# Kernel tuning notes

Hardware: AMD Instinct MI355X
Metric: run time of the kernel (lower is better)

Reference implementation:

```python
import jax, jax.numpy as jnp
import numpy as np

N_CTRL_U = 64
N_CTRL_V = 64
N_EVAL = 2001  # int(1/0.0005) + 1


def _clamped_knots(p, n_ctrl, dtype):
    """Clamped uniform knot vector on [0,1], length n_ctrl + p + 1."""
    n_internal = n_ctrl - p - 1
    internal = jnp.linspace(0.0, 1.0, n_internal + 2, dtype=dtype)[1:-1]
    return jnp.concatenate([
        jnp.zeros(p + 1, dtype=dtype), internal, jnp.ones(p + 1, dtype=dtype)
    ])


def _find_spans(knots, u, p, n_ctrl):
    """Knot-span index for each parameter (NURBS book A2.1, via searchsorted)."""
    return jnp.clip(jnp.searchsorted(knots, u, side='right') - 1, p, n_ctrl - 1)


def _basis_functions(knots, spans, u, p):
    """Cox-de-Boor nonzero basis functions (NURBS book A2.2), vectorized over u.
    Returns [N, p+1]."""
    Ns = [jnp.ones_like(u)]
    left = {}
    right = {}
    for j in range(1, p + 1):
        left[j] = u - knots[spans + 1 - j]
        right[j] = knots[spans + j] - u
        saved = jnp.zeros_like(u)
        new = []
        for r in range(j):
            temp = Ns[r] / (right[r + 1] + left[j - r])
            new.append(saved + right[r + 1] * temp)
            saved = left[j - r] * temp
        new.append(saved)
        Ns = new
    return jnp.stack(Ns, axis=-1)


def setup_inputs() -> dict:
    key = jax.random.key(0)
    k1, = jax.random.split(key, 1)
    control_points = jax.random.normal(k1, (N_CTRL_U, N_CTRL_V, 3), dtype=jnp.float32)
    params_u = jnp.linspace(0.0, 1.0, N_EVAL, dtype=jnp.float32)
    params_v = jnp.linspace(0.0, 1.0, N_EVAL, dtype=jnp.float32)
    return {"control_points": control_points, "params_u": params_u,
            "params_v": params_v, "degree": 3}


def reference(control_points, params_u, params_v, degree):
    p = int(degree)
    n_u, n_v, d = control_points.shape
    dt = control_points.dtype
    ku = _clamped_knots(p, n_u, dt)
    kv = _clamped_knots(p, n_v, dt)
    su = _find_spans(ku, params_u, p, n_u)          # [Nu]
    sv = _find_spans(kv, params_v, p, n_v)          # [Nv]
    Bu = _basis_functions(ku, su, params_u, p)      # [Nu, p+1]
    Bv = _basis_functions(kv, sv, params_v, p)      # [Nv, p+1]
    off = jnp.arange(p + 1)
    iu = su[:, None] - p + off[None, :]             # [Nu, p+1]
    iv = sv[:, None] - p + off[None, :]             # [Nv, p+1]
    # Contract u first to keep intermediates small: [Nu, p+1, n_v, d] -> [Nu, n_v, d]
    ctrl_u = control_points[iu]                     # gather rows by span
    curve_u = jnp.einsum('ua,uavd->uvd', Bu, ctrl_u)
    # Gather v spans then contract: [Nu, Nv, p+1, d] -> [Nu, Nv, d]
    pts = curve_u[:, iv]
    return jnp.einsum('vb,uvbd->uvd', Bv, pts)
```

## Files before the change

kernel.cpp:

```cpp
#include <hip/hip_runtime.h>

#define N_EVAL 2001
#define NCTRL  64

__device__ __forceinline__ float knotv(int i) {
    if (i <= 3) return 0.0f;
    if (i >= NCTRL) return 1.0f;
    return (float)(i - 3) * (1.0f / 61.0f);
}

__device__ __forceinline__ void basis_p3(float u, int& span, float4& N) {
    int s = 3 + (int)floorf(u * 61.0f);
    s = max(3, min(63, s));
    while (s < 63 && knotv(s + 1) <= u) ++s;
    while (s > 3 && knotv(s) > u) --s;

    float left[4], right[4], Ns[4];
    Ns[0] = 1.0f;
    #pragma unroll
    for (int j = 1; j <= 3; ++j) {
        left[j]  = u - knotv(s + 1 - j);
        right[j] = knotv(s + j) - u;
        float saved = 0.0f;
        #pragma unroll
        for (int r = 0; r < j; ++r) {
            float temp = Ns[r] / (right[r + 1] + left[j - r]);
            Ns[r] = saved + right[r + 1] * temp;
            saved = left[j - r] * temp;
        }
        Ns[j] = saved;
    }
    span = s;
    N = make_float4(Ns[0], Ns[1], Ns[2], Ns[3]);
}

__global__ void basis_kernel(const float* __restrict__ pu, const float* __restrict__ pv,
                             float4* __restrict__ Bu, float4* __restrict__ Bv,
                             int* __restrict__ su, int* __restrict__ sv) {
    int gid = blockIdx.x * blockDim.x + threadIdx.x;
    if (gid < 2048) {
        if (gid < N_EVAL) {
            int s; float4 N;
            basis_p3(pu[gid], s, N);
            Bu[gid] = N; su[gid] = s;
        }
    } else {
        int i = gid - 2048;
        if (i < N_EVAL) {
            int s; float4 N;
            basis_p3(pv[i], s, N);
            Bv[i] = N; sv[i] = s;
        }
    }
}

__global__ __launch_bounds__(256) void eval_kernel(const float* __restrict__ cp,
                                                   const float4* __restrict__ Bu,
                                                   const float4* __restrict__ Bv,
                                                   const int* __restrict__ su,
                                                   const int* __restrict__ sv,
                                                   float* __restrict__ out) {
    __shared__ float4 curve[NCTRL];
    __shared__ float  stage[768];

    const int u = blockIdx.x;
    const int t = threadIdx.x;
    const int s_u = su[u];
    const float4 bu = Bu[u];

    if (t < NCTRL * 3) {
        const int base = (s_u - 3) * (NCTRL * 3);
        float c = bu.x * cp[base +       t]
                + bu.y * cp[base + 192 + t]
                + bu.z * cp[base + 384 + t]
                + bu.w * cp[base + 576 + t];
        int j = t / 3, d = t - 3 * j;
        ((float*)curve)[j * 4 + d] = c;
    }
    __syncthreads();

    float* orow = out + (size_t)u * (N_EVAL * 3);

    #pragma unroll
    for (int k = 0; k < 8; ++k) {
        const int v = k * 256 + t;
        float x = 0.f, y = 0.f, z = 0.f;
        if (v < N_EVAL) {
            const float4 bv = Bv[v];
            const int iv0 = sv[v] - 3;
            float4 c0 = curve[iv0 + 0];
            float4 c1 = curve[iv0 + 1];
            float4 c2 = curve[iv0 + 2];
            float4 c3 = curve[iv0 + 3];
            x = bv.x * c0.x + bv.y * c1.x + bv.z * c2.x + bv.w * c3.x;
            y = bv.x * c0.y + bv.y * c1.y + bv.z * c2.y + bv.w * c3.y;
            z = bv.x * c0.z + bv.y * c1.z + bv.z * c2.z + bv.w * c3.z;
        }
        if (k) __syncthreads();
        if (v < N_EVAL) {
            stage[3 * t + 0] = x;
            stage[3 * t + 1] = y;
            stage[3 * t + 2] = z;
        }
        __syncthreads();
        const int rowbase = k * 768;
        #pragma unroll
        for (int j = 0; j < 3; ++j) {
            int idx = j * 256 + t;
            if (rowbase + idx < N_EVAL * 3)
                orow[rowbase + idx] = stage[idx];
        }
    }
}

extern "C" void kernel_launch(void* const* d_in, const int* in_sizes, int n_in,
                              void* d_out, int out_size, void* d_ws, size_t ws_size,
                              hipStream_t stream) {
    const float* cp = (const float*)d_in[0];
    const float* pu = (const float*)d_in[1];
    const float* pv = (const float*)d_in[2];
    float* out = (float*)d_out;

    float4* Bu = (float4*)d_ws;
    float4* Bv = Bu + 2048;
    int* su = (int*)(Bu + 4096);
    int* sv = su + 2048;

    basis_kernel<<<16, 256, 0, stream>>>(pu, pv, Bu, Bv, su, sv);
    eval_kernel<<<N_EVAL, 256, 0, stream>>>(cp, Bu, Bv, su, sv, out);
}
```

Measured before the change: 83.05 us.

## Fuse basis computation into eval kernel and vectorize aligned row stores

Drops the separate basis kernel: each block computes its u basis inline, and every thread recomputes its v basis per element rather than loading precomputed values. The output staging buffer is double-buffered, which removes one barrier per iteration, and it is shifted so each row can be written with aligned float4 stores plus scalar head and tail writes. Division is replaced by the hardware reciprocal. The cost is redundant basis arithmetic across 2001 blocks, and the approximate reciprocal may change numerics slightly.

```diff
diff --git a/kernel.cpp b/kernel.cpp
--- a/kernel.cpp
+++ b/kernel.cpp
@@ -2,6 +2,7 @@
 
 #define N_EVAL 2001
 #define NCTRL  64
+#define ROWF   (N_EVAL * 3)
 
 __device__ __forceinline__ float knotv(int i) {
     if (i <= 3) return 0.0f;
@@ -24,7 +25,7 @@
         float saved = 0.0f;
         #pragma unroll
         for (int r = 0; r < j; ++r) {
-            float temp = Ns[r] / (right[r + 1] + left[j - r]);
+            float temp = Ns[r] * __builtin_amdgcn_rcpf(right[r + 1] + left[j - r]);
             Ns[r] = saved + right[r + 1] * temp;
             saved = left[j - r] * temp;
         }
@@ -34,39 +35,18 @@
     N = make_float4(Ns[0], Ns[1], Ns[2], Ns[3]);
 }
 
-__global__ void basis_kernel(const float* __restrict__ pu, const float* __restrict__ pv,
-                             float4* __restrict__ Bu, float4* __restrict__ Bv,
-                             int* __restrict__ su, int* __restrict__ sv) {
-    int gid = blockIdx.x * blockDim.x + threadIdx.x;
-    if (gid < 2048) {
-        if (gid < N_EVAL) {
-            int s; float4 N;
-            basis_p3(pu[gid], s, N);
-            Bu[gid] = N; su[gid] = s;
-        }
-    } else {
-        int i = gid - 2048;
-        if (i < N_EVAL) {
-            int s; float4 N;
-            basis_p3(pv[i], s, N);
-            Bv[i] = N; sv[i] = s;
-        }
-    }
-}
-
 __global__ __launch_bounds__(256) void eval_kernel(const float* __restrict__ cp,
-                                                   const float4* __restrict__ Bu,
-                                                   const float4* __restrict__ Bv,
-                                                   const int* __restrict__ su,
-                                                   const int* __restrict__ sv,
+                                                   const float* __restrict__ pu,
+                                                   const float* __restrict__ pv,
                                                    float* __restrict__ out) {
     __shared__ float4 curve[NCTRL];
-    __shared__ float  stage[768];
+    __shared__ float  stage[2][776];
 
     const int u = blockIdx.x;
     const int t = threadIdx.x;
-    const int s_u = su[u];
-    const float4 bu = Bu[u];
+
+    int s_u; float4 bu;
+    basis_p3(pu[u], s_u, bu);
 
     if (t < NCTRL * 3) {
         const int base = (s_u - 3) * (NCTRL * 3);
@@ -79,15 +59,17 @@
     }
     __syncthreads();
 
-    float* orow = out + (size_t)u * (N_EVAL * 3);
+    const size_t rowstart = (size_t)u * ROWF;
+    const int shift    = (int)(rowstart & 3);
+    const int slotbase = shift ? 4 : 0;
 
-    #pragma unroll
     for (int k = 0; k < 8; ++k) {
         const int v = k * 256 + t;
         float x = 0.f, y = 0.f, z = 0.f;
         if (v < N_EVAL) {
-            const float4 bv = Bv[v];
-            const int iv0 = sv[v] - 3;
+            int s_v; float4 bv;
+            basis_p3(pv[v], s_v, bv);
+            const int iv0 = s_v - 3;
             float4 c0 = curve[iv0 + 0];
             float4 c1 = curve[iv0 + 1];
             float4 c2 = curve[iv0 + 2];
@@ -96,19 +78,33 @@
             y = bv.x * c0.y + bv.y * c1.y + bv.z * c2.y + bv.w * c3.y;
             z = bv.x * c0.z + bv.y * c1.z + bv.z * c2.z + bv.w * c3.z;
         }
-        if (k) __syncthreads();
+        float* st = stage[k & 1];
         if (v < N_EVAL) {
-            stage[3 * t + 0] = x;
-            stage[3 * t + 1] = y;
-            stage[3 * t + 2] = z;
+            st[3 * t + 0 + shift] = x;
+            st[3 * t + 1 + shift] = y;
+            st[3 * t + 2 + shift] = z;
         }
         __syncthreads();
-        const int rowbase = k * 768;
-        #pragma unroll
-        for (int j = 0; j < 3; ++j) {
-            int idx = j * 256 + t;
-            if (rowbase + idx < N_EVAL * 3)
-                orow[rowbase + idx] = stage[idx];
+
+        const int    g0    = k * 768;
+        const int    cnt   = (g0 + 768 <= ROWF) ? 768 : (ROWF - g0);
+        const size_t gabs0 = rowstart + g0;
+        const int    head  = (4 - shift) & 3;
+        const int    nf    = (cnt - head) >> 2;
+
+        if (t < nf) {
+            float4 q = *reinterpret_cast<const float4*>(&st[slotbase + 4 * t]);
+            reinterpret_cast<float4*>(out + gabs0 + head)[t] = q;
+        }
+        if (t >= 240 && t < 240 + head) {
+            int h = t - 240;
+            out[gabs0 + h] = st[shift + h];
+        }
+        const int done  = head + 4 * nf;
+        const int tailc = cnt - done;
+        if (t >= 244 && t < 244 + tailc) {
+            int h = t - 244;
+            out[gabs0 + done + h] = st[shift + done + h];
         }
     }
 }
@@ -121,11 +117,5 @@
     const float* pv = (const float*)d_in[2];
     float* out = (float*)d_out;
 
-    float4* Bu = (float4*)d_ws;
-    float4* Bv = Bu + 2048;
-    int* su = (int*)(Bu + 4096);
-    int* sv = su + 2048;
-
-    basis_kernel<<<16, 256, 0, stream>>>(pu, pv, Bu, Bv, su, sv);
-    eval_kernel<<<N_EVAL, 256, 0, stream>>>(cp, Bu, Bv, su, sv, out);
+    eval_kernel<<<N_EVAL, 256, 0, stream>>>(cp, pu, pv, out);
 }
```

Result: slower. 93.58 us (+12.7%).

## Write output rows with aligned float4 stores and pack v-basis with span

Applied to the files above, without the earlier changes.

Each output row is now written as aligned float4 vectors. Each thread recomputes the two points that straddle its 16-byte slot, and a few threads fill the unaligned head and tail elements, so the shared-memory staging buffer and its barriers go away. The v-basis is packed into one float4 holding three weights plus the span, with the fourth weight rebuilt as one minus the sum, which removes a separate span load. The cost is roughly double the point evaluations and a small floating-point difference in the rebuilt weight.

```diff
diff --git a/kernel.cpp b/kernel.cpp
--- a/kernel.cpp
+++ b/kernel.cpp
@@ -2,6 +2,7 @@
 
 #define N_EVAL 2001
 #define NCTRL  64
+#define ROWF   6003
 
 __device__ __forceinline__ float knotv(int i) {
     if (i <= 3) return 0.0f;
@@ -9,13 +10,12 @@
     return (float)(i - 3) * (1.0f / 61.0f);
 }
 
-__device__ __forceinline__ void basis_p3(float u, int& span, float4& N) {
+__device__ __forceinline__ void basis_p3(float u, int& span, float* Ns) {
     int s = 3 + (int)floorf(u * 61.0f);
     s = max(3, min(63, s));
     while (s < 63 && knotv(s + 1) <= u) ++s;
     while (s > 3 && knotv(s) > u) --s;
-
-    float left[4], right[4], Ns[4];
+    float left[4], right[4];
     Ns[0] = 1.0f;
     #pragma unroll
     for (int j = 1; j <= 3; ++j) {
@@ -31,42 +31,45 @@
         Ns[j] = saved;
     }
     span = s;
-    N = make_float4(Ns[0], Ns[1], Ns[2], Ns[3]);
 }
 
 __global__ void basis_kernel(const float* __restrict__ pu, const float* __restrict__ pv,
-                             float4* __restrict__ Bu, float4* __restrict__ Bv,
-                             int* __restrict__ su, int* __restrict__ sv) {
+                             float4* __restrict__ Bu4, int* __restrict__ su,
+                             float4* __restrict__ bvp) {
     int gid = blockIdx.x * blockDim.x + threadIdx.x;
-    if (gid < 2048) {
-        if (gid < N_EVAL) {
-            int s; float4 N;
-            basis_p3(pu[gid], s, N);
-            Bu[gid] = N; su[gid] = s;
-        }
-    } else {
-        int i = gid - 2048;
-        if (i < N_EVAL) {
-            int s; float4 N;
-            basis_p3(pv[i], s, N);
-            Bv[i] = N; sv[i] = s;
-        }
-    }
+    if (gid >= N_EVAL) return;
+    int s; float N[4];
+    basis_p3(pu[gid], s, N);
+    Bu4[gid] = make_float4(N[0], N[1], N[2], N[3]);
+    su[gid] = s;
+    int s2; float M[4];
+    basis_p3(pv[gid], s2, M);
+    bvp[gid] = make_float4(M[0], M[1], M[2], (float)s2);
+}
+
+__device__ __forceinline__ float3 eval_pt(const float4* __restrict__ curve, float4 q) {
+    float b3 = 1.0f - q.x - q.y - q.z;
+    int iv0 = (int)q.w - 3;
+    float4 c0 = curve[iv0 + 0];
+    float4 c1 = curve[iv0 + 1];
+    float4 c2 = curve[iv0 + 2];
+    float4 c3 = curve[iv0 + 3];
+    return make_float3(q.x * c0.x + q.y * c1.x + q.z * c2.x + b3 * c3.x,
+                       q.x * c0.y + q.y * c1.y + q.z * c2.y + b3 * c3.y,
+                       q.x * c0.z + q.y * c1.z + q.z * c2.z + b3 * c3.z);
 }
 
 __global__ __launch_bounds__(256) void eval_kernel(const float* __restrict__ cp,
-                                                   const float4* __restrict__ Bu,
-                                                   const float4* __restrict__ Bv,
+                                                   const float4* __restrict__ Bu4,
                                                    const int* __restrict__ su,
-                                                   const int* __restrict__ sv,
+                                                   const float4* __restrict__ bvp,
                                                    float* __restrict__ out) {
     __shared__ float4 curve[NCTRL];
-    __shared__ float  stage[768];
 
     const int u = blockIdx.x;
     const int t = threadIdx.x;
     const int s_u = su[u];
-    const float4 bu = Bu[u];
+    const float4 bu = Bu4[u];
 
     if (t < NCTRL * 3) {
         const int base = (s_u - 3) * (NCTRL * 3);
@@ -79,37 +82,41 @@
     }
     __syncthreads();
 
-    float* orow = out + (size_t)u * (N_EVAL * 3);
+    const size_t S = (size_t)u * ROWF;
+    const int shift = (int)(S & 3);
+    const int head  = (4 - shift) & 3;
+    const int tail  = 3 - head;
+    float4* outv = (float4*)(out + S + head);
 
     #pragma unroll
-    for (int k = 0; k < 8; ++k) {
-        const int v = k * 256 + t;
-        float x = 0.f, y = 0.f, z = 0.f;
-        if (v < N_EVAL) {
-            const float4 bv = Bv[v];
-            const int iv0 = sv[v] - 3;
-            float4 c0 = curve[iv0 + 0];
-            float4 c1 = curve[iv0 + 1];
-            float4 c2 = curve[iv0 + 2];
-            float4 c3 = curve[iv0 + 3];
-            x = bv.x * c0.x + bv.y * c1.x + bv.z * c2.x + bv.w * c3.x;
-            y = bv.x * c0.y + bv.y * c1.y + bv.z * c2.y + bv.w * c3.y;
-            z = bv.x * c0.z + bv.y * c1.z + bv.z * c2.z + bv.w * c3.z;
+    for (int k = 0; k < 6; ++k) {
+        const int slot = k * 256 + t;
+        if (slot < 1500) {
+            const int f  = head + 4 * slot;
+            const int v0 = f / 3;
+            const int ph = f - 3 * v0;
+            float4 q0 = bvp[v0];
+            float4 q1 = bvp[v0 + 1];
+            float3 P0 = eval_pt(curve, q0);
+            float3 P1 = eval_pt(curve, q1);
+            float4 r;
+            if (ph == 0)      r = make_float4(P0.x, P0.y, P0.z, P1.x);
+            else if (ph == 1) r = make_float4(P0.y, P0.z, P1.x, P1.y);
+            else              r = make_float4(P0.z, P1.x, P1.y, P1.z);
+            outv[slot] = r;
         }
-        if (k) __syncthreads();
-        if (v < N_EVAL) {
-            stage[3 * t + 0] = x;
-            stage[3 * t + 1] = y;
-            stage[3 * t + 2] = z;
-        }
-        __syncthreads();
-        const int rowbase = k * 768;
-        #pragma unroll
-        for (int j = 0; j < 3; ++j) {
-            int idx = j * 256 + t;
-            if (rowbase + idx < N_EVAL * 3)
-                orow[rowbase + idx] = stage[idx];
-        }
+    }
+
+    if (t >= 248 && t < 248 + head) {
+        int h = t - 248;
+        float3 P = eval_pt(curve, bvp[0]);
+        out[S + h] = (h == 0) ? P.x : (h == 1 ? P.y : P.z);
+    }
+    if (t >= 252 && t < 252 + tail) {
+        int h = t - 252;
+        float3 P = eval_pt(curve, bvp[2000]);
+        int comp = 3 - tail + h;
+        out[S + ROWF - tail + h] = (comp == 0) ? P.x : (comp == 1 ? P.y : P.z);
     }
 }
 
@@ -121,11 +128,10 @@
     const float* pv = (const float*)d_in[2];
     float* out = (float*)d_out;
 
-    float4* Bu = (float4*)d_ws;
-    float4* Bv = Bu + 2048;
-    int* su = (int*)(Bu + 4096);
-    int* sv = su + 2048;
+    float4* Bu4 = (float4*)d_ws;
+    float4* bvp = Bu4 + N_EVAL;
+    int* su = (int*)(bvp + N_EVAL);
 
-    basis_kernel<<<16, 256, 0, stream>>>(pu, pv, Bu, Bv, su, sv);
-    eval_kernel<<<N_EVAL, 256, 0, stream>>>(cp, Bu, Bv, su, sv, out);
+    basis_kernel<<<8, 256, 0, stream>>>(pu, pv, Bu4, su, bvp);
+    eval_kernel<<<N_EVAL, 256, 0, stream>>>(cp, Bu4, su, bvp, out);
 }
```

Result: no change. 82.85 us (-0.2%).
